# Kernel tuning notes

Measured on AMD Instinct MI355X. Metric: run time of the kernel, lower is better.

Reference implementation:

```python
import jax, jax.numpy as jnp
import numpy as np
from jax import lax

_CLIP_MIN = 1e-06
_CLIP_MAX = 1.0
_POS_ALPHA = 0.0005
NUM_CLASSES = 21
RADIUS = 3
HALF_D = RADIUS * RADIUS
POOL = 3
PAD = POOL // 2
IGNORE = 255
LAM = 0.5  # loss_weight_lambda, lambda_way=1


def _max_pool(x):
    # NCHW max pool, kernel=stride=3, padding=1
    return lax.reduce_window(x, -jnp.inf, lax.max,
                             (1, 1, POOL, POOL), (1, 1, POOL, POOL),
                             ((0, 0), (0, 0), (PAD, PAD), (PAD, PAD)))


def _get_pairs(x):
    # stack radius*radius shifted crops -> [N, C, r^2, nh, nw]
    h, w = x.shape[2], x.shape[3]
    nh, nw = h - RADIUS + 1, w - RADIUS + 1
    crops = [x[:, :, y:y + nh, xo:xo + nw] for y in range(RADIUS) for xo in range(RADIUS)]
    return jnp.stack(crops, axis=2)


def _log_det_by_cholesky(m):
    chol = jnp.linalg.cholesky(m)
    return 2.0 * jnp.sum(jnp.log(jnp.diagonal(chol, axis1=-2, axis2=-1) + 1e-08), axis=-1)


def _rmi_lower_bound(labels_4d, probs_4d):
    la = _max_pool(labels_4d)
    pr = _max_pool(probs_4d)
    n, c = la.shape[0], la.shape[1]
    la_v = _get_pairs(la).reshape(n, c, HALF_D, -1)   # [N,C,d,L]
    pr_v = _get_pairs(pr).reshape(n, c, HALF_D, -1)
    la_v = la_v - jnp.mean(la_v, axis=3, keepdims=True)
    pr_v = pr_v - jnp.mean(pr_v, axis=3, keepdims=True)
    la_cov = jnp.einsum('ncdl,ncel->ncde', la_v, la_v)
    pr_cov = jnp.einsum('ncdl,ncel->ncde', pr_v, pr_v)
    eye = jnp.eye(HALF_D, dtype=la_cov.dtype)
    pr_cov_inv = jnp.linalg.inv(pr_cov + eye * _POS_ALPHA)
    la_pr_cov = jnp.einsum('ncdl,ncel->ncde', la_v, pr_v)
    appro_var = la_cov - jnp.einsum('ncde,ncef,ncgf->ncdg', la_pr_cov, pr_cov_inv, la_pr_cov)
    rmi_now = 0.5 * _log_det_by_cholesky(appro_var + eye * _POS_ALPHA)  # [N,C]
    rmi_per_class = jnp.mean(rmi_now.reshape(-1, NUM_CLASSES), axis=0) / float(HALF_D)
    return jnp.sum(rmi_per_class)


def setup_inputs() -> dict:
    key = jax.random.key(0)
    k1, k2 = jax.random.split(key)
    score = jax.random.normal(k1, (4, NUM_CLASSES, 512, 512), dtype=jnp.float32)
    target = jax.random.randint(k2, (4, 512, 512), 0, NUM_CLASSES, dtype=jnp.int64)
    return {"score": score, "target": target}


def reference(score, target):
    # cross entropy with ignore_index=255, mean reduction
    logp = jax.nn.log_softmax(score, axis=1)                      # [N,C,H,W]
    valid_ce = (target != IGNORE)
    safe_t = jnp.where(valid_ce, target, 0)
    nll = -jnp.take_along_axis(logp, safe_t[:, None].astype(jnp.int32), axis=1)[:, 0]
    normal_loss = jnp.sum(jnp.where(valid_ce, nll, 0.0)) / jnp.sum(valid_ce.astype(jnp.float32))

    # valid one-hot labels and masked sigmoid probs
    mask = (target < NUM_CLASSES)                                 # [N,H,W]
    maskf = mask.astype(jnp.float32)
    onehot = jax.nn.one_hot((target * mask).astype(jnp.int32), NUM_CLASSES, dtype=jnp.float32)
    onehot = onehot * maskf[..., None]                            # [N,H,W,C]
    onehot = jnp.transpose(onehot, (0, 3, 1, 2))                  # [N,C,H,W]
    probs = jnp.clip(jax.nn.sigmoid(score) * maskf[:, None], _CLIP_MIN, _CLIP_MAX)

    rmi_loss = _rmi_lower_bound(onehot, probs)
    return LAM * normal_loss + rmi_loss * (1.0 - LAM)
```

## Files before the change

### kernel.cpp

```cpp
#include <hip/hip_runtime.h>
#include <cfloat>
#include <cmath>

#define DEVINL __device__ __forceinline__

constexpr int N_ = 4, C_ = 21, H_ = 512, W_ = 512;
constexpr int P_ = 171;
constexpr int Q_ = 169;
constexpr int NC_ = N_ * C_;
constexpr int HW_ = H_ * W_;
constexpr int PP_ = P_ * P_;
constexpr int NCOV_ = 189;
constexpr float EPS_ = 5e-4f;

DEVINL constexpr int tstart(int d) { return d * 9 - d * (d - 1) / 2; }

DEVINL float wave_sum(float v) {
#pragma unroll
    for (int o = 32; o > 0; o >>= 1) v += __shfl_down(v, o, 64);
    return v;
}

__global__ __launch_bounds__(256) void k_fused(const float* __restrict__ score,
                                               const int* __restrict__ target,
                                               float* __restrict__ pr,
                                               float* __restrict__ la,
                                               float* __restrict__ cov_ce) {
    __shared__ float sP[C_][W_];
    __shared__ unsigned sM[W_];
    int bid = blockIdx.x;
    int i = bid % P_;
    int n = bid / P_;
    const float* sbase = score + (size_t)n * C_ * HW_;
    const int* tbase = target + (size_t)n * HW_;
    int h0 = 3 * i - 1;
    int hlo = h0 < 0 ? 0 : h0;
    int hhi = h0 + 2;

    float nll = 0.f, cnt = 0.f;
    for (int w = threadIdx.x; w < W_; w += 256) {
        float vmax[C_];
#pragma unroll
        for (int c = 0; c < C_; ++c) vmax[c] = 0.f;
        unsigned lm = 0;
        for (int h = hlo; h <= hhi; ++h) {
            const float* sp = sbase + (size_t)h * W_ + w;
            int t = tbase[h * W_ + w];
            float s[C_];
#pragma unroll
            for (int c = 0; c < C_; ++c) s[c] = sp[(size_t)c * HW_];
            float m = s[0];
#pragma unroll
            for (int c = 1; c < C_; ++c) m = fmaxf(m, s[c]);
            float se = 0.f;
#pragma unroll
            for (int c = 0; c < C_; ++c) se += __expf(s[c] - m);
            float lse = m + __logf(se);
            if (t != 255) {
                int tc = (t >= 0 && t < C_) ? t : 0;
                nll += (lse - s[tc]);
                cnt += 1.f;
            }
            bool mv = (t >= 0 && t < C_);
            if (mv) lm |= (1u << t);
            float mf = mv ? 1.f : 0.f;
#pragma unroll
            for (int c = 0; c < C_; ++c) {
                float p = mf * __builtin_amdgcn_rcpf(1.f + __expf(-s[c]));
                vmax[c] = fmaxf(vmax[c], p);
            }
        }
#pragma unroll
        for (int c = 0; c < C_; ++c) sP[c][w] = vmax[c];
        sM[w] = lm;
    }
    __syncthreads();

    size_t ob = (size_t)n * C_ * PP_ + (size_t)i * P_;
    for (int item = threadIdx.x; item < C_ * P_; item += 256) {
        int c = item / P_;
        int j = item - c * P_;
        int w0 = 3 * j - 1;
        int wl = w0 < 0 ? 0 : w0;
        int wh = w0 + 2 > W_ - 1 ? W_ - 1 : w0 + 2;
        float m = 0.f;
        unsigned bits = 0;
        for (int w = wl; w <= wh; ++w) {
            m = fmaxf(m, sP[c][w]);
            bits |= sM[w];
        }
        m = fminf(fmaxf(m, 1e-6f), 1.f);
        pr[ob + (size_t)c * PP_ + j] = m;
        la[ob + (size_t)c * PP_ + j] = ((bits >> c) & 1u) ? 1.f : 0.f;
    }

    nll = wave_sum(nll);
    cnt = wave_sum(cnt);
    if ((threadIdx.x & 63) == 0) {
        atomicAdd(&cov_ce[NC_ * NCOV_ + 0], nll);
        atomicAdd(&cov_ce[NC_ * NCOV_ + 1], cnt);
    }
}

__global__ __launch_bounds__(256, 2) void k_cov(const float* __restrict__ la,
                                                const float* __restrict__ pr,
                                                float* __restrict__ cov) {
    int nc = blockIdx.x;
    int chunk = blockIdx.y;
    const float* A = la + (size_t)nc * PP_;
    const float* B = pr + (size_t)nc * PP_;
    constexpr int RC = 29;
    int r0 = chunk * RC;
    int rend = r0 + RC;
    if (rend > Q_) rend = Q_;
    int npts = (rend - r0) * Q_;

    float sA[9], sB[9], SAA[45], SBB[45], SAB[81];
#pragma unroll
    for (int k = 0; k < 9; ++k) { sA[k] = 0.f; sB[k] = 0.f; }
#pragma unroll
    for (int k = 0; k < 45; ++k) { SAA[k] = 0.f; SBB[k] = 0.f; }
#pragma unroll
    for (int k = 0; k < 81; ++k) SAB[k] = 0.f;

    for (int idx = threadIdx.x; idx < npts; idx += 256) {
        int lr = idx / Q_;
        int col = idx - lr * Q_;
        int row = r0 + lr;
        const float* ap = A + row * P_ + col;
        const float* bp = B + row * P_ + col;
        float a[9], b[9];
#pragma unroll
        for (int dy = 0; dy < 3; ++dy)
#pragma unroll
            for (int dx = 0; dx < 3; ++dx) {
                a[dy * 3 + dx] = ap[dy * P_ + dx];
                b[dy * 3 + dx] = bp[dy * P_ + dx];
            }
#pragma unroll
        for (int d = 0; d < 9; ++d) { sA[d] += a[d]; sB[d] += b[d]; }
        {
            int k = 0;
#pragma unroll
            for (int d = 0; d < 9; ++d)
#pragma unroll
                for (int e = d; e < 9; ++e) {
                    SAA[k] += a[d] * a[e];
                    SBB[k] += b[d] * b[e];
                    ++k;
                }
        }
#pragma unroll
        for (int d = 0; d < 9; ++d)
#pragma unroll
            for (int e = 0; e < 9; ++e) SAB[d * 9 + e] += a[d] * b[e];
    }

    __shared__ float red[4][NCOV_];
    int lane = threadIdx.x & 63;
    int wv = threadIdx.x >> 6;
#pragma unroll
    for (int d = 0; d < 9; ++d) { float v = wave_sum(sA[d]); if (lane == 0) red[wv][d] = v; }
#pragma unroll
    for (int d = 0; d < 9; ++d) { float v = wave_sum(sB[d]); if (lane == 0) red[wv][9 + d] = v; }
#pragma unroll
    for (int k = 0; k < 45; ++k) { float v = wave_sum(SAA[k]); if (lane == 0) red[wv][18 + k] = v; }
#pragma unroll
    for (int k = 0; k < 45; ++k) { float v = wave_sum(SBB[k]); if (lane == 0) red[wv][63 + k] = v; }
#pragma unroll
    for (int k = 0; k < 81; ++k) { float v = wave_sum(SAB[k]); if (lane == 0) red[wv][108 + k] = v; }
    __syncthreads();
    for (int k = threadIdx.x; k < NCOV_; k += 256) {
        float v = red[0][k] + red[1][k] + red[2][k] + red[3][k];
        atomicAdd(&cov[nc * NCOV_ + k], v);
    }
}

__global__ __launch_bounds__(128) void k_final(const float* __restrict__ cov,
                                               float* __restrict__ out) {
    __shared__ float red[128];
    int t = threadIdx.x;
    float my = 0.f;
    if (t < NC_) {
        const float* S = cov + t * NCOV_;
        const float Lf = (float)(Q_ * Q_);
        float sA[9], sB[9];
#pragma unroll
        for (int d = 0; d < 9; ++d) { sA[d] = S[d]; sB[d] = S[9 + d]; }
        float laC[45], M[45], Cm[81];
        {
            int k = 0;
#pragma unroll
            for (int d = 0; d < 9; ++d)
#pragma unroll
                for (int e = d; e < 9; ++e) {
                    laC[k] = S[18 + k] - sA[d] * sA[e] / Lf;
                    M[k] = S[63 + k] - sB[d] * sB[e] / Lf + (d == e ? EPS_ : 0.f);
                    ++k;
                }
#pragma unroll
            for (int d = 0; d < 9; ++d)
#pragma unroll
                for (int e = 0; e < 9; ++e)
                    Cm[d * 9 + e] = S[108 + d * 9 + e] - sA[d] * sB[e] / Lf;
        }
#pragma unroll
        for (int j = 0; j < 9; ++j) {
            float s = M[tstart(j)];
#pragma unroll
            for (int k = 0; k < j; ++k) { float l = M[tstart(k) + (j - k)]; s -= l * l; }
            float dj = sqrtf(fmaxf(s, 1e-30f));
            M[tstart(j)] = dj;
            float inv = 1.f / dj;
#pragma unroll
            for (int i = j + 1; i < 9; ++i) {
                float s2 = M[tstart(j) + (i - j)];
#pragma unroll
                for (int k = 0; k < j; ++k)
                    s2 -= M[tstart(k) + (i - k)] * M[tstart(k) + (j - k)];
                M[tstart(j) + (i - j)] = s2 * inv;
            }
        }
#pragma unroll
        for (int p = 0; p < 9; ++p) {
#pragma unroll
            for (int i = 0; i < 9; ++i) {
                float s = Cm[p * 9 + i];
#pragma unroll
                for (int k = 0; k < i; ++k)
                    s -= M[tstart(k) + (i - k)] * Cm[p * 9 + k];
                Cm[p * 9 + i] = s / M[tstart(i)];
            }
        }
#pragma unroll
        for (int d = 0; d < 9; ++d)
#pragma unroll
            for (int e = d; e < 9; ++e) {
                float s = 0.f;
#pragma unroll
                for (int i = 0; i < 9; ++i) s += Cm[d * 9 + i] * Cm[e * 9 + i];
                laC[tstart(d) + (e - d)] -= s;
                if (d == e) laC[tstart(d)] += EPS_;
            }
        float rmi = 0.f;
#pragma unroll
        for (int j = 0; j < 9; ++j) {
            float s = laC[tstart(j)];
#pragma unroll
            for (int k = 0; k < j; ++k) { float l = laC[tstart(k) + (j - k)]; s -= l * l; }
            float dj = sqrtf(fmaxf(s, 0.f));
            laC[tstart(j)] = dj;
            float inv = 1.f / fmaxf(dj, 1e-30f);
#pragma unroll
            for (int i = j + 1; i < 9; ++i) {
                float s2 = laC[tstart(j) + (i - j)];
#pragma unroll
                for (int k = 0; k < j; ++k)
                    s2 -= laC[tstart(k) + (i - k)] * laC[tstart(k) + (j - k)];
                laC[tstart(j) + (i - j)] = s2 * inv;
            }
            rmi += __logf(dj + 1e-8f);
        }
        my = rmi;
    }
    red[t] = my;
    __syncthreads();
#pragma unroll
    for (int o = 64; o > 0; o >>= 1) {
        if (t < o) red[t] += red[t + o];
        __syncthreads();
    }
    if (t == 0) {
        float rmi_total = red[0] / 36.f;
        float ce = cov[NC_ * NCOV_ + 0] / cov[NC_ * NCOV_ + 1];
        out[0] = 0.5f * ce + 0.5f * rmi_total;
    }
}

extern "C" void kernel_launch(void* const* d_in, const int* in_sizes, int n_in,
                              void* d_out, int out_size, void* d_ws, size_t ws_size,
                              hipStream_t stream) {
    const float* score = (const float*)d_in[0];
    const int* target = (const int*)d_in[1];
    float* pr = (float*)d_ws;
    float* la = pr + (size_t)NC_ * PP_;
    float* cov = la + (size_t)NC_ * PP_;
    hipMemsetAsync(cov, 0, (size_t)(NC_ * NCOV_ + 2) * sizeof(float), stream);

    k_fused<<<dim3(N_ * P_), dim3(256), 0, stream>>>(score, target, pr, la, cov);
    dim3 g2(NC_, 6);
    k_cov<<<g2, dim3(256), 0, stream>>>(la, pr, cov);
    k_final<<<dim3(1), dim3(128), 0, stream>>>(cov, (float*)d_out);
}
```

Measured before the change: 282.3 us.

## Widen fused block, share exp between softmax and sigmoid, split covariance accumulation

The fused kernel now runs 512 threads so each thread handles exactly one column, and it computes sigmoid from the same exp used for the softmax (E/(E+exp(-m))), which removes the second exp per class. The covariance kernel gains a third grid dimension that splits the AA, BB and AB accumulators into separate blocks. This lowers register pressure and allows higher occupancy (launch bounds raised to 4). The cost is reading the la/pr inputs multiple times and issuing more atomics.

```diff
diff --git a/kernel.cpp b/kernel.cpp
--- a/kernel.cpp
+++ b/kernel.cpp
@@ -12,6 +12,7 @@
 constexpr int PP_ = P_ * P_;
 constexpr int NCOV_ = 189;
 constexpr float EPS_ = 5e-4f;
+constexpr int RC_ = 29;
 
 DEVINL constexpr int tstart(int d) { return d * 9 - d * (d - 1) / 2; }
 
@@ -21,11 +22,11 @@
     return v;
 }
 
-__global__ __launch_bounds__(256) void k_fused(const float* __restrict__ score,
-                                               const int* __restrict__ target,
-                                               float* __restrict__ pr,
-                                               float* __restrict__ la,
-                                               float* __restrict__ cov_ce) {
+__global__ __launch_bounds__(512, 6) void k_fused(const float* __restrict__ score,
+                                                  const int* __restrict__ target,
+                                                  float* __restrict__ pr,
+                                                  float* __restrict__ la,
+                                                  float* __restrict__ cov_ce) {
     __shared__ float sP[C_][W_];
     __shared__ unsigned sM[W_];
     int bid = blockIdx.x;
@@ -37,60 +38,61 @@
     int hlo = h0 < 0 ? 0 : h0;
     int hhi = h0 + 2;
 
+    int w = threadIdx.x;
+    float vmax[C_];
+#pragma unroll
+    for (int c = 0; c < C_; ++c) vmax[c] = 0.f;
+    unsigned lm = 0;
     float nll = 0.f, cnt = 0.f;
-    for (int w = threadIdx.x; w < W_; w += 256) {
-        float vmax[C_];
-#pragma unroll
-        for (int c = 0; c < C_; ++c) vmax[c] = 0.f;
-        unsigned lm = 0;
-        for (int h = hlo; h <= hhi; ++h) {
-            const float* sp = sbase + (size_t)h * W_ + w;
-            int t = tbase[h * W_ + w];
-            float s[C_];
-#pragma unroll
-            for (int c = 0; c < C_; ++c) s[c] = sp[(size_t)c * HW_];
-            float m = s[0];
-#pragma unroll
-            for (int c = 1; c < C_; ++c) m = fmaxf(m, s[c]);
-            float se = 0.f;
-#pragma unroll
-            for (int c = 0; c < C_; ++c) se += __expf(s[c] - m);
-            float lse = m + __logf(se);
-            if (t != 255) {
-                int tc = (t >= 0 && t < C_) ? t : 0;
-                nll += (lse - s[tc]);
-                cnt += 1.f;
-            }
-            bool mv = (t >= 0 && t < C_);
-            if (mv) lm |= (1u << t);
-            float mf = mv ? 1.f : 0.f;
-#pragma unroll
-            for (int c = 0; c < C_; ++c) {
-                float p = mf * __builtin_amdgcn_rcpf(1.f + __expf(-s[c]));
-                vmax[c] = fmaxf(vmax[c], p);
-            }
-        }
-#pragma unroll
-        for (int c = 0; c < C_; ++c) sP[c][w] = vmax[c];
-        sM[w] = lm;
-    }
+
+    for (int h = hlo; h <= hhi; ++h) {
+        const float* sp = sbase + (size_t)h * W_ + w;
+        int t = tbase[h * W_ + w];
+        float s[C_];
+#pragma unroll
+        for (int c = 0; c < C_; ++c) s[c] = sp[(size_t)c * HW_];
+        float m = s[0];
+#pragma unroll
+        for (int c = 1; c < C_; ++c) m = fmaxf(m, s[c]);
+        float K = __expf(-m);
+        bool mv = (t >= 0 && t < C_);
+        float mf = mv ? 1.f : 0.f;
+        if (mv) lm |= (1u << t);
+        int tc = (t != 255) ? ((t >= 0 && t < C_) ? t : 0) : -1;
+        float se = 0.f, stgt = 0.f;
+#pragma unroll
+        for (int c = 0; c < C_; ++c) {
+            float E = __expf(s[c] - m);
+            se += E;
+            if (c == tc) stgt = s[c];
+            float p = mf * E * __builtin_amdgcn_rcpf(E + K);
+            vmax[c] = fmaxf(vmax[c], p);
+        }
+        if (tc >= 0) {
+            nll += (m + __logf(se) - stgt);
+            cnt += 1.f;
+        }
+    }
+#pragma unroll
+    for (int c = 0; c < C_; ++c) sP[c][w] = vmax[c];
+    sM[w] = lm;
     __syncthreads();
 
     size_t ob = (size_t)n * C_ * PP_ + (size_t)i * P_;
-    for (int item = threadIdx.x; item < C_ * P_; item += 256) {
+    for (int item = threadIdx.x; item < C_ * P_; item += 512) {
         int c = item / P_;
         int j = item - c * P_;
         int w0 = 3 * j - 1;
         int wl = w0 < 0 ? 0 : w0;
         int wh = w0 + 2 > W_ - 1 ? W_ - 1 : w0 + 2;
-        float m = 0.f;
+        float mx = 0.f;
         unsigned bits = 0;
-        for (int w = wl; w <= wh; ++w) {
-            m = fmaxf(m, sP[c][w]);
-            bits |= sM[w];
-        }
-        m = fminf(fmaxf(m, 1e-6f), 1.f);
-        pr[ob + (size_t)c * PP_ + j] = m;
+        for (int ww = wl; ww <= wh; ++ww) {
+            mx = fmaxf(mx, sP[c][ww]);
+            bits |= sM[ww];
+        }
+        mx = fminf(fmaxf(mx, 1e-6f), 1.f);
+        pr[ob + (size_t)c * PP_ + j] = mx;
         la[ob + (size_t)c * PP_ + j] = ((bits >> c) & 1u) ? 1.f : 0.f;
     }
 
@@ -102,77 +104,88 @@
     }
 }
 
-__global__ __launch_bounds__(256, 2) void k_cov(const float* __restrict__ la,
+__global__ __launch_bounds__(256, 4) void k_cov(const float* __restrict__ la,
                                                 const float* __restrict__ pr,
                                                 float* __restrict__ cov) {
     int nc = blockIdx.x;
     int chunk = blockIdx.y;
-    const float* A = la + (size_t)nc * PP_;
-    const float* B = pr + (size_t)nc * PP_;
-    constexpr int RC = 29;
-    int r0 = chunk * RC;
-    int rend = r0 + RC;
+    int part = blockIdx.z;
+    int r0 = chunk * RC_;
+    int rend = r0 + RC_;
     if (rend > Q_) rend = Q_;
     int npts = (rend - r0) * Q_;
 
-    float sA[9], sB[9], SAA[45], SBB[45], SAB[81];
-#pragma unroll
-    for (int k = 0; k < 9; ++k) { sA[k] = 0.f; sB[k] = 0.f; }
-#pragma unroll
-    for (int k = 0; k < 45; ++k) { SAA[k] = 0.f; SBB[k] = 0.f; }
-#pragma unroll
-    for (int k = 0; k < 81; ++k) SAB[k] = 0.f;
-
-    for (int idx = threadIdx.x; idx < npts; idx += 256) {
-        int lr = idx / Q_;
-        int col = idx - lr * Q_;
-        int row = r0 + lr;
-        const float* ap = A + row * P_ + col;
-        const float* bp = B + row * P_ + col;
-        float a[9], b[9];
-#pragma unroll
-        for (int dy = 0; dy < 3; ++dy)
-#pragma unroll
-            for (int dx = 0; dx < 3; ++dx) {
-                a[dy * 3 + dx] = ap[dy * P_ + dx];
-                b[dy * 3 + dx] = bp[dy * P_ + dx];
-            }
-#pragma unroll
-        for (int d = 0; d < 9; ++d) { sA[d] += a[d]; sB[d] += b[d]; }
-        {
-            int k = 0;
-#pragma unroll
-            for (int d = 0; d < 9; ++d)
-#pragma unroll
-                for (int e = d; e < 9; ++e) {
-                    SAA[k] += a[d] * a[e];
-                    SBB[k] += b[d] * b[e];
-                    ++k;
-                }
-        }
-#pragma unroll
-        for (int d = 0; d < 9; ++d)
-#pragma unroll
-            for (int e = 0; e < 9; ++e) SAB[d * 9 + e] += a[d] * b[e];
-    }
-
-    __shared__ float red[4][NCOV_];
+    __shared__ float red[4][81];
     int lane = threadIdx.x & 63;
     int wv = threadIdx.x >> 6;
-#pragma unroll
-    for (int d = 0; d < 9; ++d) { float v = wave_sum(sA[d]); if (lane == 0) red[wv][d] = v; }
-#pragma unroll
-    for (int d = 0; d < 9; ++d) { float v = wave_sum(sB[d]); if (lane == 0) red[wv][9 + d] = v; }
-#pragma unroll
-    for (int k = 0; k < 45; ++k) { float v = wave_sum(SAA[k]); if (lane == 0) red[wv][18 + k] = v; }
-#pragma unroll
-    for (int k = 0; k < 45; ++k) { float v = wave_sum(SBB[k]); if (lane == 0) red[wv][63 + k] = v; }
-#pragma unroll
-    for (int k = 0; k < 81; ++k) { float v = wave_sum(SAB[k]); if (lane == 0) red[wv][108 + k] = v; }
-    __syncthreads();
-    for (int k = threadIdx.x; k < NCOV_; k += 256) {
-        float v = red[0][k] + red[1][k] + red[2][k] + red[3][k];
-        atomicAdd(&cov[nc * NCOV_ + k], v);
+
+    if (part < 2) {
+        const float* X = (part == 0 ? la : pr) + (size_t)nc * PP_;
+        float s1[9], s2[45];
+#pragma unroll
+        for (int k = 0; k < 9; ++k) s1[k] = 0.f;
+#pragma unroll
+        for (int k = 0; k < 45; ++k) s2[k] = 0.f;
+        for (int idx = threadIdx.x; idx < npts; idx += 256) {
+            int lr = idx / Q_;
+            int col = idx - lr * Q_;
+            const float* xp = X + (r0 + lr) * P_ + col;
+            float a[9];
+#pragma unroll
+            for (int dy = 0; dy < 3; ++dy)
+#pragma unroll
+                for (int dx = 0; dx < 3; ++dx) a[dy * 3 + dx] = xp[dy * P_ + dx];
+#pragma unroll
+            for (int d = 0; d < 9; ++d) s1[d] += a[d];
+            int k = 0;
+#pragma unroll
+            for (int d = 0; d < 9; ++d)
+#pragma unroll
+                for (int e = d; e < 9; ++e) { s2[k] += a[d] * a[e]; ++k; }
+        }
+#pragma unroll
+        for (int k = 0; k < 9; ++k) { float v = wave_sum(s1[k]); if (lane == 0) red[wv][k] = v; }
+#pragma unroll
+        for (int k = 0; k < 45; ++k) { float v = wave_sum(s2[k]); if (lane == 0) red[wv][9 + k] = v; }
+        __syncthreads();
+        int b1 = (part == 0) ? 0 : 9;
+        int b2 = (part == 0) ? 18 : 63;
+        for (int k = threadIdx.x; k < 54; k += 256) {
+            float v = red[0][k] + red[1][k] + red[2][k] + red[3][k];
+            int dst = (k < 9) ? (b1 + k) : (b2 + k - 9);
+            atomicAdd(&cov[nc * NCOV_ + dst], v);
+        }
+    } else {
+        const float* A = la + (size_t)nc * PP_;
+        const float* B = pr + (size_t)nc * PP_;
+        float sab[81];
+#pragma unroll
+        for (int k = 0; k < 81; ++k) sab[k] = 0.f;
+        for (int idx = threadIdx.x; idx < npts; idx += 256) {
+            int lr = idx / Q_;
+            int col = idx - lr * Q_;
+            const float* ap = A + (r0 + lr) * P_ + col;
+            const float* bp = B + (r0 + lr) * P_ + col;
+            float a[9], b[9];
+#pragma unroll
+            for (int dy = 0; dy < 3; ++dy)
+#pragma unroll
+                for (int dx = 0; dx < 3; ++dx) {
+                    a[dy * 3 + dx] = ap[dy * P_ + dx];
+                    b[dy * 3 + dx] = bp[dy * P_ + dx];
+                }
+#pragma unroll
+            for (int d = 0; d < 9; ++d)
+#pragma unroll
+                for (int e = 0; e < 9; ++e) sab[d * 9 + e] += a[d] * b[e];
+        }
+#pragma unroll
+        for (int k = 0; k < 81; ++k) { float v = wave_sum(sab[k]); if (lane == 0) red[wv][k] = v; }
+        __syncthreads();
+        for (int k = threadIdx.x; k < 81; k += 256) {
+            float v = red[0][k] + red[1][k] + red[2][k] + red[3][k];
+            atomicAdd(&cov[nc * NCOV_ + 108 + k], v);
+        }
     }
 }
 
@@ -287,8 +300,7 @@
     float* cov = la + (size_t)NC_ * PP_;
     hipMemsetAsync(cov, 0, (size_t)(NC_ * NCOV_ + 2) * sizeof(float), stream);
 
-    k_fused<<<dim3(N_ * P_), dim3(256), 0, stream>>>(score, target, pr, la, cov);
-    dim3 g2(NC_, 6);
-    k_cov<<<g2, dim3(256), 0, stream>>>(la, pr, cov);
+    k_fused<<<dim3(N_ * P_), dim3(512), 0, stream>>>(score, target, pr, la, cov);
+    k_cov<<<dim3(NC_, 6, 3), dim3(256), 0, stream>>>(la, pr, cov);
     k_final<<<dim3(1), dim3(128), 0, stream>>>(cov, (float*)d_out);
 }
```

Result: slower. 344.3 us (+22.0%).
